# Kernel optimization log

Measured on AMD Instinct MI355X. Metric: run time of the kernel, lower is better.

## Reference

```python
import jax, jax.numpy as jnp
import numpy as np

# ---- static module config (matches torch defaults) ----
N_LEVELS = 16
MIN_RES = 16
MAX_RES = 512
N_ENC = 2 ** 14
D = 3          # n_input_dims
E = 2          # n_embed_dims
B = 1 << 20    # number of query points

# per-level resolutions, computed in float32 to mirror torch's float32 log/exp
_gf = np.exp((np.log(np.float32(MAX_RES)) - np.log(np.float32(MIN_RES))) / np.float32(N_LEVELS - 1)).astype(np.float32)
RES = [int(np.floor(np.float32(MIN_RES) * _gf ** np.float32(l))) for l in range(N_LEVELS)]
DIRECT = [r ** D < N_ENC for r in RES]                  # small grids use direct ravel indexing
NLE = [min(r ** D, N_ENC) for r in RES]                  # encodings per level (sentinel row at index NLE[l])

# 2^D corner offsets, shape (8, 3)
OFFS = np.stack(np.meshgrid(*([np.arange(2)] * D), indexing='ij'), axis=-1).reshape(-1, D).astype(np.int32)
# instant-ngp spatial hashing primes
PRIMES = (1, 2654435761, 805459861)


def setup_inputs() -> dict:
    key = jax.random.key(0)
    k1, k2 = jax.random.split(key)
    x = jax.random.uniform(k1, (B, D), dtype=jnp.float32, minval=-1.0, maxval=1.0)
    # stacked per-level tables, padded to (N_ENC+1, E); rows >= NLE[l] zeroed
    emb = jax.random.uniform(k2, (N_LEVELS, N_ENC + 1, E), dtype=jnp.float32, minval=-1e-4, maxval=1e-4)
    row = np.arange(N_ENC + 1)
    valid = (row[None, :] < np.asarray(NLE)[:, None])    # (L, N_ENC+1); also zeroes the sentinel row
    emb = emb * jnp.asarray(valid[..., None], dtype=jnp.float32)
    return {"x": x, "emb": emb}


def _level_features(x, emb_l, R, n_encs, direct):
    offs = jnp.asarray(OFFS)                             # (8, 3)
    xs = (x + 1.0) * (R * 0.5) - 0.5                     # grid coords
    xl = jnp.floor(xs)
    frac = xs - xl                                       # (B, 3)
    xi = xl.astype(jnp.int32)
    c = xi[:, None, :] + offs[None, :, :]                # (B, 8, 3) corner indices
    # bilinear/trilinear weights: prod over dims of frac (offset=1) or 1-frac (offset=0)
    w = jnp.prod(jnp.where(offs[None].astype(bool), frac[:, None, :], 1.0 - frac[:, None, :]), axis=-1)  # (B, 8)
    w = jax.lax.stop_gradient(w)                         # torch computes weights under no_grad
    m = jnp.all((c >= 0) & (c < R), axis=-1)             # (B, 8) corner validity
    if direct:
        ids = (c[..., 0] * R + c[..., 1]) * R + c[..., 2]
    else:
        cu = c.astype(jnp.uint32)
        h = (cu[..., 0] * jnp.uint32(PRIMES[0])
             ^ cu[..., 1] * jnp.uint32(PRIMES[1])
             ^ cu[..., 2] * jnp.uint32(PRIMES[2]))
        ids = (h % jnp.uint32(n_encs)).astype(jnp.int32)
    ids = jnp.where(m, ids, n_encs)                      # invalid corners -> zero sentinel row
    return jnp.sum(emb_l[ids] * w[..., None], axis=1)    # (B, E)


def reference(x, emb):
    feats = [
        _level_features(x, emb[l], RES[l], NLE[l], DIRECT[l])
        for l in range(N_LEVELS)
    ]
    return jnp.stack(feats, axis=1)                      # (B, L, E)
```

## Files before the change

### kernel.cpp

```cpp
#include <hip/hip_runtime.h>


#define B_POINTS (1 << 20)
#define N_LEVELS 16
#define TAB_F2   16385
#define WG       1024
#define CHUNK    8192
#define PPT      (CHUNK / WG)
#define NCHUNK   (B_POINTS / CHUNK)
#define NWG      (NCHUNK * N_LEVELS)

__constant__ int   cRES[N_LEVELS]  = {16, 20, 25, 32, 40, 50, 64, 80,
                                      101, 128, 161, 203, 256, 322, 406, 512};
__constant__ float cHALF[N_LEVELS] = {8.f, 10.f, 12.5f, 16.f, 20.f, 25.f, 32.f, 40.f,
                                      50.5f, 64.f, 80.5f, 101.5f, 128.f, 161.f, 203.f, 256.f};
__constant__ int   cSENT[N_LEVELS] = {4096, 8000, 15625, 16384, 16384, 16384, 16384, 16384,
                                      16384, 16384, 16384, 16384, 16384, 16384, 16384, 16384};

__global__ __launch_bounds__(WG)
void hashenc_lds(const float* __restrict__ x,
                 const float* __restrict__ emb,
                 float* __restrict__ out)
{
    __shared__ float2 tab[TAB_F2];

    const int bid = blockIdx.x;
    const int xcd = bid & 7;
    const int s   = bid >> 3;
    const int l   = s & 15;
    const int c   = ((s >> 4) << 3) | xcd;

    const int   R    = cRES[l];
    const float half = cHALF[l];
    const int   sent = cSENT[l];
    const bool  direct = (l < 3);

    const float2* __restrict__ g = (const float2*)emb + (size_t)l * TAB_F2;
    const int t = threadIdx.x;
#pragma unroll
    for (int j = 0; j < 16; ++j)
        tab[j * WG + t] = g[j * WG + t];
    if (t == 0) tab[16384] = g[16384];
    __syncthreads();

    const int base = c * CHUNK;
#pragma unroll
    for (int k = 0; k < PPT; ++k) {
        const int p = base + k * WG + t;

        const float x0 = x[p * 3 + 0];
        const float x1 = x[p * 3 + 1];
        const float x2 = x[p * 3 + 2];

        const float xs0 = (x0 + 1.0f) * half - 0.5f;
        const float xs1 = (x1 + 1.0f) * half - 0.5f;
        const float xs2 = (x2 + 1.0f) * half - 0.5f;
        const float fl0 = floorf(xs0), fl1 = floorf(xs1), fl2 = floorf(xs2);
        const float f0 = xs0 - fl0, f1 = xs1 - fl1, f2 = xs2 - fl2;
        const float g0 = 1.0f - f0, g1 = 1.0f - f1, g2 = 1.0f - f2;
        const int i0 = (int)fl0, i1 = (int)fl1, i2 = (int)fl2;

        float acc0 = 0.0f, acc1 = 0.0f;
#pragma unroll
        for (int q = 0; q < 8; ++q) {
            const int o0 = (q >> 2) & 1, o1 = (q >> 1) & 1, o2 = q & 1;
            const int c0 = i0 + o0, c1 = i1 + o1, c2 = i2 + o2;
            const float w = (o0 ? f0 : g0) * (o1 ? f1 : g1) * (o2 ? f2 : g2);
            const bool valid = (c0 >= 0) & (c0 < R) &
                               (c1 >= 0) & (c1 < R) &
                               (c2 >= 0) & (c2 < R);
            int id;
            if (direct) {
                id = (c0 * R + c1) * R + c2;
            } else {
                const unsigned h = (unsigned)c0 * 1u
                                 ^ (unsigned)c1 * 2654435761u
                                 ^ (unsigned)c2 * 805459861u;
                id = (int)(h & 16383u);
            }
            id = valid ? id : sent;
            const float2 e = tab[id];
            acc0 = fmaf(e.x, w, acc0);
            acc1 = fmaf(e.y, w, acc1);
        }

        ((float2*)out)[(size_t)p * N_LEVELS + l] = make_float2(acc0, acc1);
    }
}

extern "C" void kernel_launch(void* const* d_in, const int* in_sizes, int n_in,
                              void* d_out, int out_size, void* d_ws, size_t ws_size,
                              hipStream_t stream) {
    const float* x   = (const float*)d_in[0];
    const float* emb = (const float*)d_in[1];
    float* out = (float*)d_out;

    hashenc_lds<<<NWG, WG, 0, stream>>>(x, emb, out);
}
```

Baseline: 240.1 us.

## Factor corner weights and hashes per axis, fold validity into weights, use fewer workgroups

Per-axis validity masks are folded into the separable weights, so invalid corners get zero weight instead of being redirected to a sentinel row. Direct indices are clamped so they stay in range. Hash and index terms are computed per axis and shared across the 8 corners. Accumulation uses a 2-wide vector type that may lower to packed FMA. The grid shrinks to 512 workgroups, each handling more points with a partial unroll, so the per-workgroup LDS table load is amortised over more work at the cost of fewer concurrent workgroups. Results can differ slightly if a table entry is non-finite, since a zero weight no longer selects the zero sentinel row.

```diff
diff --git a/kernel.cpp b/kernel.cpp
--- a/kernel.cpp
+++ b/kernel.cpp
@@ -1,28 +1,28 @@
 #include <hip/hip_runtime.h>
 
+
+typedef __attribute__((ext_vector_type(2))) float f32x2;
 
 #define B_POINTS (1 << 20)
 #define N_LEVELS 16
 #define TAB_F2   16385
 #define WG       1024
-#define CHUNK    8192
+#define NWG      512
+#define NCHUNK   (NWG / N_LEVELS)
+#define CHUNK    (B_POINTS / NCHUNK)
 #define PPT      (CHUNK / WG)
-#define NCHUNK   (B_POINTS / CHUNK)
-#define NWG      (NCHUNK * N_LEVELS)
 
 __constant__ int   cRES[N_LEVELS]  = {16, 20, 25, 32, 40, 50, 64, 80,
                                       101, 128, 161, 203, 256, 322, 406, 512};
 __constant__ float cHALF[N_LEVELS] = {8.f, 10.f, 12.5f, 16.f, 20.f, 25.f, 32.f, 40.f,
                                       50.5f, 64.f, 80.5f, 101.5f, 128.f, 161.f, 203.f, 256.f};
-__constant__ int   cSENT[N_LEVELS] = {4096, 8000, 15625, 16384, 16384, 16384, 16384, 16384,
-                                      16384, 16384, 16384, 16384, 16384, 16384, 16384, 16384};
 
 __global__ __launch_bounds__(WG)
 void hashenc_lds(const float* __restrict__ x,
                  const float* __restrict__ emb,
                  float* __restrict__ out)
 {
-    __shared__ float2 tab[TAB_F2];
+    __shared__ f32x2 tab[TAB_F2];
 
     const int bid = blockIdx.x;
     const int xcd = bid & 7;
@@ -30,21 +30,20 @@
     const int l   = s & 15;
     const int c   = ((s >> 4) << 3) | xcd;
 
-    const int   R    = cRES[l];
-    const float half = cHALF[l];
-    const int   sent = cSENT[l];
+    const int   R      = cRES[l];
+    const float half   = cHALF[l];
     const bool  direct = (l < 3);
 
-    const float2* __restrict__ g = (const float2*)emb + (size_t)l * TAB_F2;
+    const f32x2* __restrict__ gtab = (const f32x2*)emb + (size_t)l * TAB_F2;
     const int t = threadIdx.x;
 #pragma unroll
     for (int j = 0; j < 16; ++j)
-        tab[j * WG + t] = g[j * WG + t];
-    if (t == 0) tab[16384] = g[16384];
+        tab[j * WG + t] = gtab[j * WG + t];
+    if (t == 0) tab[16384] = gtab[16384];
     __syncthreads();
 
     const int base = c * CHUNK;
-#pragma unroll
+#pragma unroll 2
     for (int k = 0; k < PPT; ++k) {
         const int p = base + k * WG + t;
 
@@ -60,31 +59,45 @@
         const float g0 = 1.0f - f0, g1 = 1.0f - f1, g2 = 1.0f - f2;
         const int i0 = (int)fl0, i1 = (int)fl1, i2 = (int)fl2;
 
-        float acc0 = 0.0f, acc1 = 0.0f;
-#pragma unroll
-        for (int q = 0; q < 8; ++q) {
-            const int o0 = (q >> 2) & 1, o1 = (q >> 1) & 1, o2 = q & 1;
-            const int c0 = i0 + o0, c1 = i1 + o1, c2 = i2 + o2;
-            const float w = (o0 ? f0 : g0) * (o1 ? f1 : g1) * (o2 ? f2 : g2);
-            const bool valid = (c0 >= 0) & (c0 < R) &
-                               (c1 >= 0) & (c1 < R) &
-                               (c2 >= 0) & (c2 < R);
-            int id;
-            if (direct) {
-                id = (c0 * R + c1) * R + c2;
-            } else {
-                const unsigned h = (unsigned)c0 * 1u
-                                 ^ (unsigned)c1 * 2654435761u
-                                 ^ (unsigned)c2 * 805459861u;
-                id = (int)(h & 16383u);
-            }
-            id = valid ? id : sent;
-            const float2 e = tab[id];
-            acc0 = fmaf(e.x, w, acc0);
-            acc1 = fmaf(e.y, w, acc1);
+        const float wx0 = ((i0     >= 0) && (i0     < R)) ? g0 : 0.0f;
+        const float wx1 = ((i0 + 1 >= 0) && (i0 + 1 < R)) ? f0 : 0.0f;
+        const float wy0 = ((i1     >= 0) && (i1     < R)) ? g1 : 0.0f;
+        const float wy1 = ((i1 + 1 >= 0) && (i1 + 1 < R)) ? f1 : 0.0f;
+        const float wz0 = ((i2     >= 0) && (i2     < R)) ? g2 : 0.0f;
+        const float wz1 = ((i2 + 1 >= 0) && (i2 + 1 < R)) ? f2 : 0.0f;
+
+        const float pxy00 = wx0 * wy0, pxy01 = wx0 * wy1;
+        const float pxy10 = wx1 * wy0, pxy11 = wx1 * wy1;
+        const float w[8] = {pxy00 * wz0, pxy00 * wz1, pxy01 * wz0, pxy01 * wz1,
+                            pxy10 * wz0, pxy10 * wz1, pxy11 * wz0, pxy11 * wz1};
+
+        int id[8];
+        if (direct) {
+            const int Rm1 = R - 1;
+            const int u0l = min(max(i0,     0), Rm1), u0h = min(max(i0 + 1, 0), Rm1);
+            const int u1l = min(max(i1,     0), Rm1), u1h = min(max(i1 + 1, 0), Rm1);
+            const int u2l = min(max(i2,     0), Rm1), u2h = min(max(i2 + 1, 0), Rm1);
+            const int a0  = u0l * R, a1 = u0h * R;
+            const int b00 = (a0 + u1l) * R, b01 = (a0 + u1h) * R;
+            const int b10 = (a1 + u1l) * R, b11 = (a1 + u1h) * R;
+            id[0] = b00 + u2l; id[1] = b00 + u2h; id[2] = b01 + u2l; id[3] = b01 + u2h;
+            id[4] = b10 + u2l; id[5] = b10 + u2h; id[6] = b11 + u2l; id[7] = b11 + u2h;
+        } else {
+            const unsigned hx0 = (unsigned)i0,                   hx1 = (unsigned)(i0 + 1);
+            const unsigned hy0 = (unsigned)i1 * 2654435761u,     hy1 = (unsigned)(i1 + 1) * 2654435761u;
+            const unsigned hz0 = (unsigned)i2 * 805459861u,      hz1 = (unsigned)(i2 + 1) * 805459861u;
+            id[0] = (int)((hx0 ^ hy0 ^ hz0) & 16383u); id[1] = (int)((hx0 ^ hy0 ^ hz1) & 16383u);
+            id[2] = (int)((hx0 ^ hy1 ^ hz0) & 16383u); id[3] = (int)((hx0 ^ hy1 ^ hz1) & 16383u);
+            id[4] = (int)((hx1 ^ hy0 ^ hz0) & 16383u); id[5] = (int)((hx1 ^ hy0 ^ hz1) & 16383u);
+            id[6] = (int)((hx1 ^ hy1 ^ hz0) & 16383u); id[7] = (int)((hx1 ^ hy1 ^ hz1) & 16383u);
         }
 
-        ((float2*)out)[(size_t)p * N_LEVELS + l] = make_float2(acc0, acc1);
+        f32x2 acc = {0.0f, 0.0f};
+#pragma unroll
+        for (int q = 0; q < 8; ++q)
+            acc += tab[id[q]] * w[q];
+
+        ((f32x2*)out)[(size_t)p * N_LEVELS + l] = acc;
     }
 }
 
```

Result: faster. 225.2 us (-6.2%).
